# Kernel tuning notes

Hardware: AMD Instinct MI355X
Metric: run time of the kernel (lower is better)

## Reference

```python
import jax, jax.numpy as jnp
import numpy as np

NEG = -1e30  # effective -inf that stays stable in fp32 log-sum-exp
BLANK = 0


def _lse3(a, b, c):
    m = jnp.maximum(jnp.maximum(a, b), c)
    return m + jnp.log(jnp.exp(a - m) + jnp.exp(b - m) + jnp.exp(c - m))


def _ctc_loss_sum(log_probs, input_lengths, targets, target_lengths):
    # log_probs: [B, T, V] already log-softmaxed; targets: [B, S] int, blank=0
    B, T, V = log_probs.shape
    S = targets.shape[1]
    L = 2 * S + 1  # extended label seq: blank-interleaved

    ext = jnp.full((B, L), BLANK, dtype=targets.dtype)
    ext = ext.at[:, 1::2].set(targets)  # [B, L]

    # gather per-frame log-probs of extended labels: [B, T, L]
    lp_ext = jnp.take_along_axis(
        log_probs, jnp.broadcast_to(ext[:, None, :], (B, T, L)), axis=2)

    # skip transition s-2 -> s allowed iff ext[s] != blank and ext[s] != ext[s-2]
    ext_prev2 = jnp.pad(ext[:, :-2], ((0, 0), (2, 0)), constant_values=BLANK)
    can_skip = (ext != BLANK) & (ext != ext_prev2) & (jnp.arange(L)[None, :] >= 2)

    # alpha init at t=0
    alpha = jnp.full((B, L), NEG, dtype=log_probs.dtype)
    alpha = alpha.at[:, 0].set(lp_ext[:, 0, 0])
    alpha = alpha.at[:, 1].set(lp_ext[:, 0, 1])

    lp_seq = jnp.swapaxes(lp_ext, 0, 1)[1:]          # [T-1, B, L]
    valid = jnp.arange(1, T)[:, None] < input_lengths[None, :]  # [T-1, B]

    def step(a, xs):
        lp_t, v = xs  # [B, L], [B]
        a1 = jnp.pad(a[:, :-1], ((0, 0), (1, 0)), constant_values=NEG)
        a2 = jnp.pad(a[:, :-2], ((0, 0), (2, 0)), constant_values=NEG)
        a2 = jnp.where(can_skip, a2, NEG)
        new = _lse3(a, a1, a2) + lp_t
        a = jnp.where(v[:, None], new, a)  # freeze past each utterance's length
        return a, None

    alpha, _ = jax.lax.scan(step, alpha, (lp_seq, valid))

    # terminal states: last blank (2*tl) and last label (2*tl - 1)
    end = 2 * target_lengths.astype(jnp.int32)
    aT = jnp.take_along_axis(alpha, jnp.stack([end, end - 1], axis=1), axis=1)  # [B, 2]
    ll = jax.scipy.special.logsumexp(aT, axis=1)
    loss = -ll
    loss = jnp.where(loss > 1e29, 0.0, loss)  # zero_infinity=True
    return jnp.sum(loss)  # reduction='sum'


def setup_inputs() -> dict:
    B, T, V, S = 64, 1024, 512, 128
    key = jax.random.key(0)
    k1, k2, k3, k4 = jax.random.split(key, 4)
    output_tensor = jax.random.normal(k1, (B, T, V), dtype=jnp.float32)
    output_lengths = jax.random.randint(k2, (B,), T // 2, T + 1, dtype=jnp.int32)
    target_tensor = jax.random.randint(k3, (B, S), 1, V, dtype=jnp.int32)  # no blanks
    target_lengths = jax.random.randint(k4, (B,), S // 2, S + 1, dtype=jnp.int32)
    return {"output_tensor": output_tensor, "output_lengths": output_lengths,
            "target_tensor": target_tensor, "target_lengths": target_lengths}


def reference(output_tensor, output_lengths, target_tensor, target_lengths):
    log_probs = jax.nn.log_softmax(output_tensor, axis=2)
    return _ctc_loss_sum(log_probs, output_lengths, target_tensor, target_lengths)
```

## Files before the change

kernel.cpp:

```cpp
#include <hip/hip_runtime.h>
#include <cstdint>

#define T_LEN 1024
#define V_DIM 512
#define S_LEN 128
#define NEG2  (-1.0e30f)
#define CH    32

__device__ float2 g_plab[(size_t)64 * T_LEN * 64 + 64];
__device__ float  g_pblank[(size_t)64 * T_LEN + 64];

static __device__ __forceinline__ void dma16(const void* g, void* l) {
    __builtin_amdgcn_global_load_lds(
        (const __attribute__((address_space(1))) unsigned int*)g,
        (__attribute__((address_space(3))) unsigned int*)l,
        16, 0, 0);
}

static __device__ __forceinline__ float dpp_shr1_f(float x) {
    return __int_as_float(__builtin_amdgcn_update_dpp(
        0, __float_as_int(x), 0x138, 0xF, 0xF, true));
}
static __device__ __forceinline__ int dpp_shr1_i(int x) {
    return __builtin_amdgcn_update_dpp(0, x, 0x138, 0xF, 0xF, true);
}
template <int CTRL>
static __device__ __forceinline__ float dpp_add(float x) {
    const int y = __builtin_amdgcn_update_dpp(0, __float_as_int(x), CTRL, 0xF, 0xF, true);
    return x + __int_as_float(y);
}

__global__ __launch_bounds__(256) void ctc_prep(
    const float* __restrict__ x, const int* __restrict__ lens,
    const int* __restrict__ tgts)
{
    const int lane = threadIdx.x & 63;
    const int wid  = (int)((blockIdx.x * blockDim.x + threadIdx.x) >> 6);
    const int b = wid >> 10;
    const int t = wid & (T_LEN - 1);
    if (t >= lens[b]) return;

    const float* row = x + (size_t)wid * V_DIM;
    const float4 u = *(const float4*)(row + lane * 8);
    const float4 v = *(const float4*)(row + lane * 8 + 4);

    const float L2E = 1.44269504088896340736f;
    float s = exp2f(u.x * L2E) + exp2f(u.y * L2E)
            + exp2f(u.z * L2E) + exp2f(u.w * L2E)
            + exp2f(v.x * L2E) + exp2f(v.y * L2E)
            + exp2f(v.z * L2E) + exp2f(v.w * L2E);
    s = dpp_add<0x111>(s);
    s = dpp_add<0x112>(s);
    s = dpp_add<0x114>(s);
    s = dpp_add<0x118>(s);
    s = dpp_add<0x142>(s);
    s = dpp_add<0x143>(s);
    const float off =
        log2f(__int_as_float(__builtin_amdgcn_readlane(__float_as_int(s), 63)));

    if (lane == 0) g_pblank[wid] = exp2f(u.x * L2E - off);

    const int2 tg = *(const int2*)(tgts + b * S_LEN + 2 * lane);
    g_plab[(size_t)wid * 64 + lane] =
        make_float2(exp2f(row[tg.x] * L2E - off), exp2f(row[tg.y] * L2E - off));
}

struct AlphaState { float a0, a1, a2, a3, a4; int C; };

static __device__ __forceinline__ void alpha_step(
    AlphaState& st, float pb, float2 lp, float cs1f, float cs3f, bool dead)
{
    const float p3 = dpp_shr1_f(st.a3);
    const int   Cp = dpp_shr1_i(st.C);
    const int   Cn = dead ? Cp : st.C;
    int e = 127 + (Cp - Cn);
    e = e < 0 ? 0 : (e > 252 ? 252 : e);
    const float adj = __int_as_float((unsigned)e << 23);
    const float p3v = p3 * adj;
    const float s01 = st.a0 + st.a1;
    const float s23 = st.a2 + st.a3;
    const float n0 = (st.a0 + p3v) * pb;
    const float n1 = fmaf(p3v, cs1f, s01) * lp.x;
    const float n2 = (st.a1 + st.a2) * pb;
    const float n3 = fmaf(st.a1, cs3f, s23) * lp.y;
    const float n4 = (st.a3 + st.a4) * pb;
    st.a0 = n0; st.a1 = n1; st.a2 = n2; st.a3 = n3; st.a4 = n4; st.C = Cn;
}

static __device__ __forceinline__ void alpha_rescale(AlphaState& st)
{
    const float mx = fmaxf(fmaxf(fmaxf(st.a0, st.a1), fmaxf(st.a2, st.a3)), st.a4);
    const int ee = (__float_as_int(mx) >> 23) & 255;
    const bool ok = (ee > 0) && (ee < 255);
    const float sc = ok ? __int_as_float((unsigned)(254 - ee) << 23) : 1.0f;
    const int dC = ok ? (ee - 127) : 0;
    st.a0 *= sc; st.a1 *= sc; st.a2 *= sc; st.a3 *= sc; st.a4 *= sc; st.C += dC;
}

__global__ __launch_bounds__(64) void ctc_alpha(
    const int* __restrict__ lens, const int* __restrict__ tgts,
    const int* __restrict__ tlens, float* __restrict__ out)
{
    __shared__ alignas(16) float lds_pbs[T_LEN];
    __shared__ float2 lds_pl[3][CH * 64];

    const int b    = blockIdx.x;
    const int lane = threadIdx.x;
    const int len  = lens[b];
    const int tl   = tlens[b];
    const int lenm1 = len - 1;

    const int tA = tgts[b * S_LEN + 2 * lane];
    const int tB = tgts[b * S_LEN + 2 * lane + 1];
    const int tPrev = __shfl_up(tB, 1);
    const bool cs1 = (lane > 0) && (tA != tPrev);
    const bool cs3 = (tB != tA);
    const float cs1f = cs1 ? 1.0f : 0.0f;
    const float cs3f = cs3 ? 1.0f : 0.0f;

    const int repOwn = ((lane > 0 && tA == tPrev) ? 1 : 0) + ((tB == tA) ? 1 : 0);
    int ps = repOwn;
    #pragma unroll
    for (int d = 1; d < 64; d <<= 1) {
        const int y = __shfl_up(ps, d);
        if (lane >= d) ps += y;
    }
    const int deadline = 2 * lane + (ps - repOwn);

    const size_t rowb = (size_t)b * T_LEN;
    const float*  __restrict__ pb_b = g_pblank + rowb;
    const float2* __restrict__ pl_b = g_plab + rowb * 64;

    #pragma unroll
    for (int j = 0; j < CH / 2; ++j)
        dma16(pl_b + (size_t)(1 + 2 * j) * 64 + lane * 2, &lds_pl[0][j * 128]);
    #pragma unroll
    for (int j = 0; j < CH / 2; ++j)
        dma16(pl_b + (size_t)(33 + 2 * j) * 64 + lane * 2, &lds_pl[1][j * 128]);

    #pragma unroll
    for (int k = 0; k < T_LEN / 64; ++k)
        lds_pbs[k * 64 + lane] = pb_b[k * 64 + lane + 1];

    AlphaState st;
    st.a0 = 0.f; st.a1 = 0.f; st.a2 = 0.f; st.a3 = 0.f; st.a4 = 0.f; st.C = 0;
    if (lane == 0) { st.a0 = pb_b[0]; st.a1 = pl_b[0].x; }

    int cur = 0;
    int t0 = 1;
    for (; t0 + CH <= len; t0 += CH) {
        __builtin_amdgcn_s_waitcnt(0x4F70);
        float4 pbq[CH / 4];
        #pragma unroll
        for (int j = 0; j < CH / 4; ++j)
            pbq[j] = *(const float4*)&lds_pbs[(t0 - 1) + 4 * j];
        const float* pbr = (const float*)pbq;
        float2 pl[CH];
        #pragma unroll
        for (int i = 0; i < CH; ++i)
            pl[i] = lds_pl[cur][i * 64 + lane];
        int fill = cur + 2; if (fill >= 3) fill -= 3;
        #pragma unroll
        for (int j = 0; j < CH / 2; ++j) {
            int r = t0 + 2 * CH + 2 * j;
            r = (r < lenm1) ? r : lenm1;
            dma16(pl_b + (size_t)r * 64 + lane * 2, &lds_pl[fill][j * 128]);
        }
        #pragma unroll
        for (int i = 0; i < CH; ++i) {
            const bool dead = (deadline >= t0 + i);
            alpha_step(st, pbr[i], pl[i], cs1f, cs3f, dead);
            if ((i & 3) == 3) alpha_rescale(st);
        }
        cur = (cur == 2) ? 0 : cur + 1;
    }
    __builtin_amdgcn_s_waitcnt(0x0F70);
    for (int i = 0; t0 + i < len; ++i) {
        const float2 plv = lds_pl[cur][i * 64 + lane];
        const float  pb  = lds_pbs[t0 + i - 1];
        const bool dead = (deadline >= t0 + i);
        alpha_step(st, pb, plv, cs1f, cs3f, dead);
        if ((i & 3) == 3) alpha_rescale(st);
    }

    const int end = 2 * tl;
    float v1, v2; int C1, C2;
    {
        int s = end;
        int lsrc = s >> 2; if (lsrc > 63) lsrc = 63;
        const int slot = s & 3;
        float cand = (slot == 0) ? st.a0 : (slot == 1) ? st.a1
                   : (slot == 2) ? st.a2 : st.a3;
        if (s == 256) cand = st.a4;
        v1 = __shfl(cand, lsrc);
        C1 = __shfl(st.C, lsrc);

        s = end - 1;
        lsrc = s >> 2;
        const int slot2 = s & 3;
        cand = (slot2 == 0) ? st.a0 : (slot2 == 1) ? st.a1
             : (slot2 == 2) ? st.a2 : st.a3;
        v2 = __shfl(cand, lsrc);
        C2 = __shfl(st.C, lsrc);
    }
    const float l1 = (v1 > 0.f) ? log2f(v1) + (float)C1 : NEG2;
    const float l2 = (v2 > 0.f) ? log2f(v2) + (float)C2 : NEG2;
    const float mM = fmaxf(l1, l2);
    const float ll2 = mM + log2f(exp2f(l1 - mM) + exp2f(l2 - mM));
    float loss = -ll2 * 0.69314718055994530942f;
    if (!(loss < 1e29f)) loss = 0.f;
    if (lane == 0) atomicAdd(out, loss);
}

extern "C" void kernel_launch(void* const* d_in, const int* in_sizes, int n_in,
                              void* d_out, int out_size, void* d_ws, size_t ws_size,
                              hipStream_t stream) {
    const float* x     = (const float*)d_in[0];
    const int*   lens  = (const int*)d_in[1];
    const int*   tgts  = (const int*)d_in[2];
    const int*   tlens = (const int*)d_in[3];
    float* out = (float*)d_out;

    (void)hipMemsetAsync(d_out, 0, (size_t)out_size * sizeof(float), stream);
    ctc_prep<<<(64 * T_LEN) / 4, 256, 0, stream>>>(x, lens, tgts);
    ctc_alpha<<<64, 64, 0, stream>>>(lens, tgts, tlens, out);
}
```

Measured before the change: 257.0 us.

## Fuse prep and alpha into one producer-consumer kernel with per-group flags

Merges the log-softmax/gather prep kernel and the serial alpha recursion into one launch. The first 64 blocks are consumers that run the CTC recursion, and the remaining blocks are producers that write probabilities in time-major order and bump per-(64-frame group, batch) counters. Consumers spin on these counters before prefetching chunks, so the recursion can overlap with the bandwidth-bound prep instead of waiting for all of it to finish. The blank probabilities are now also streamed per chunk instead of preloaded whole. The cost is an extra memset, atomics and spin-waits. The scheme depends on consumer blocks being scheduled first to avoid deadlock, and on producers finishing in roughly time order.

```diff
diff --git a/kernel.cpp b/kernel.cpp
--- a/kernel.cpp
+++ b/kernel.cpp
@@ -4,11 +4,17 @@
 #define T_LEN 1024
 #define V_DIM 512
 #define S_LEN 128
+#define NB    64
+#define NGRP  16
 #define NEG2  (-1.0e30f)
 #define CH    32
-
-__device__ float2 g_plab[(size_t)64 * T_LEN * 64 + 64];
-__device__ float  g_pblank[(size_t)64 * T_LEN + 64];
+#define CONS_BLOCKS 64
+#define PROD_BLOCKS 16384
+
+__device__ __align__(16) float2 g_plab[(size_t)NB * T_LEN * 64 + 64];
+__device__ __align__(16) float  g_pbs[(size_t)NB * T_LEN + 64];
+__device__ float    g_pb0[NB];
+__device__ unsigned g_flags[NGRP * NB];
 
 static __device__ __forceinline__ void dma16(const void* g, void* l) {
     __builtin_amdgcn_global_load_lds(
@@ -30,17 +36,25 @@
     return x + __int_as_float(y);
 }
 
-__global__ __launch_bounds__(256) void ctc_prep(
+static __device__ __forceinline__ void produce(
     const float* __restrict__ x, const int* __restrict__ lens,
-    const int* __restrict__ tgts)
+    const int* __restrict__ tgts, int pbid)
 {
     const int lane = threadIdx.x & 63;
-    const int wid  = (int)((blockIdx.x * blockDim.x + threadIdx.x) >> 6);
-    const int b = wid >> 10;
-    const int t = wid & (T_LEN - 1);
-    if (t >= lens[b]) return;
-
-    const float* row = x + (size_t)wid * V_DIM;
+    const int wvid = pbid * 4 + (int)(threadIdx.x >> 6);
+    const int t = wvid >> 6;
+    const int b = wvid & (NB - 1);
+    unsigned* flag = &g_flags[(t >> 6) * NB + b];
+
+    if (t >= lens[b]) {
+        if (lane == 0)
+            __hip_atomic_fetch_add(flag, 1u, __ATOMIC_RELAXED,
+                                   __HIP_MEMORY_SCOPE_AGENT);
+        return;
+    }
+
+    const size_t rowid = (size_t)b * T_LEN + t;
+    const float* row = x + rowid * V_DIM;
     const float4 u = *(const float4*)(row + lane * 8);
     const float4 v = *(const float4*)(row + lane * 8 + 4);
 
@@ -58,11 +72,27 @@
     const float off =
         log2f(__int_as_float(__builtin_amdgcn_readlane(__float_as_int(s), 63)));
 
-    if (lane == 0) g_pblank[wid] = exp2f(u.x * L2E - off);
+    if (lane == 0) {
+        const float pv = exp2f(u.x * L2E - off);
+        if (t == 0)
+            __hip_atomic_store(&g_pb0[b], pv, __ATOMIC_RELAXED,
+                               __HIP_MEMORY_SCOPE_AGENT);
+        else
+            __hip_atomic_store(&g_pbs[rowid - 1], pv, __ATOMIC_RELAXED,
+                               __HIP_MEMORY_SCOPE_AGENT);
+    }
 
     const int2 tg = *(const int2*)(tgts + b * S_LEN + 2 * lane);
-    g_plab[(size_t)wid * 64 + lane] =
-        make_float2(exp2f(row[tg.x] * L2E - off), exp2f(row[tg.y] * L2E - off));
+    union { float2 f; unsigned long long q; } cv;
+    cv.f = make_float2(exp2f(row[tg.x] * L2E - off),
+                       exp2f(row[tg.y] * L2E - off));
+    __hip_atomic_store((unsigned long long*)&g_plab[rowid * 64 + lane], cv.q,
+                       __ATOMIC_RELAXED, __HIP_MEMORY_SCOPE_AGENT);
+
+    asm volatile("s_waitcnt vmcnt(0)" ::: "memory");
+    if (lane == 0)
+        __hip_atomic_fetch_add(flag, 1u, __ATOMIC_RELAXED,
+                               __HIP_MEMORY_SCOPE_AGENT);
 }
 
 struct AlphaState { float a0, a1, a2, a3, a4; int C; };
@@ -97,14 +127,26 @@
     st.a0 *= sc; st.a1 *= sc; st.a2 *= sc; st.a3 *= sc; st.a4 *= sc; st.C += dC;
 }
 
-__global__ __launch_bounds__(64) void ctc_alpha(
+static __device__ __forceinline__ void wait_groups(int b, int& gdone, int gneed)
+{
+    if (gneed <= gdone) return;
+    do {
+        ++gdone;
+        while (__hip_atomic_load(&g_flags[gdone * NB + b], __ATOMIC_RELAXED,
+                                 __HIP_MEMORY_SCOPE_AGENT) < 64u)
+            __builtin_amdgcn_s_sleep(2);
+    } while (gdone < gneed);
+    __builtin_amdgcn_fence(__ATOMIC_ACQUIRE, "agent");
+    gdone = gneed;
+}
+
+static __device__ void consume(
     const int* __restrict__ lens, const int* __restrict__ tgts,
-    const int* __restrict__ tlens, float* __restrict__ out)
-{
-    __shared__ alignas(16) float lds_pbs[T_LEN];
-    __shared__ float2 lds_pl[3][CH * 64];
-
-    const int b    = blockIdx.x;
+    const int* __restrict__ tlens, float* __restrict__ out, int b)
+{
+    __shared__ alignas(16) float2 lds_pl[3][CH * 64];
+    __shared__ alignas(16) float  lds_pbc[3][CH];
+
     const int lane = threadIdx.x;
     const int len  = lens[b];
     const int tl   = tlens[b];
@@ -128,37 +170,42 @@
     const int deadline = 2 * lane + (ps - repOwn);
 
     const size_t rowb = (size_t)b * T_LEN;
-    const float*  __restrict__ pb_b = g_pblank + rowb;
-    const float2* __restrict__ pl_b = g_plab + rowb * 64;
+    const float*  __restrict__ pbs_b = g_pbs + rowb;
+    const float2* __restrict__ pl_b  = g_plab + rowb * 64;
+
+    int gdone = -1;
+    wait_groups(b, gdone, 1);
 
     #pragma unroll
     for (int j = 0; j < CH / 2; ++j)
         dma16(pl_b + (size_t)(1 + 2 * j) * 64 + lane * 2, &lds_pl[0][j * 128]);
+    if (lane < 8) dma16(pbs_b + lane * 4, &lds_pbc[0][0]);
     #pragma unroll
     for (int j = 0; j < CH / 2; ++j)
         dma16(pl_b + (size_t)(33 + 2 * j) * 64 + lane * 2, &lds_pl[1][j * 128]);
-
-    #pragma unroll
-    for (int k = 0; k < T_LEN / 64; ++k)
-        lds_pbs[k * 64 + lane] = pb_b[k * 64 + lane + 1];
+    if (lane < 8) dma16(pbs_b + 32 + lane * 4, &lds_pbc[1][0]);
 
     AlphaState st;
     st.a0 = 0.f; st.a1 = 0.f; st.a2 = 0.f; st.a3 = 0.f; st.a4 = 0.f; st.C = 0;
-    if (lane == 0) { st.a0 = pb_b[0]; st.a1 = pl_b[0].x; }
+    if (lane == 0) { st.a0 = g_pb0[b]; st.a1 = pl_b[0].x; }
 
     int cur = 0;
     int t0 = 1;
     for (; t0 + CH <= len; t0 += CH) {
-        __builtin_amdgcn_s_waitcnt(0x4F70);
+        __builtin_amdgcn_s_waitcnt(0x4F71);
         float4 pbq[CH / 4];
         #pragma unroll
         for (int j = 0; j < CH / 4; ++j)
-            pbq[j] = *(const float4*)&lds_pbs[(t0 - 1) + 4 * j];
+            pbq[j] = *(const float4*)&lds_pbc[cur][4 * j];
         const float* pbr = (const float*)pbq;
         float2 pl[CH];
         #pragma unroll
         for (int i = 0; i < CH; ++i)
             pl[i] = lds_pl[cur][i * 64 + lane];
+        {
+            const int gneed = ((t0 + 95 < lenm1) ? t0 + 95 : lenm1) >> 6;
+            wait_groups(b, gdone, gneed);
+        }
         int fill = cur + 2; if (fill >= 3) fill -= 3;
         #pragma unroll
         for (int j = 0; j < CH / 2; ++j) {
@@ -166,6 +213,7 @@
             r = (r < lenm1) ? r : lenm1;
             dma16(pl_b + (size_t)r * 64 + lane * 2, &lds_pl[fill][j * 128]);
         }
+        if (lane < 8) dma16(pbs_b + (t0 + 63) + lane * 4, &lds_pbc[fill][0]);
         #pragma unroll
         for (int i = 0; i < CH; ++i) {
             const bool dead = (deadline >= t0 + i);
@@ -177,7 +225,7 @@
     __builtin_amdgcn_s_waitcnt(0x0F70);
     for (int i = 0; t0 + i < len; ++i) {
         const float2 plv = lds_pl[cur][i * 64 + lane];
-        const float  pb  = lds_pbs[t0 + i - 1];
+        const float  pb  = lds_pbc[cur][i];
         const bool dead = (deadline >= t0 + i);
         alpha_step(st, pb, plv, cs1f, cs3f, dead);
         if ((i & 3) == 3) alpha_rescale(st);
@@ -212,16 +260,34 @@
     if (lane == 0) atomicAdd(out, loss);
 }
 
+__global__ __launch_bounds__(256) void ctc_fused(
+    const float* __restrict__ x, const int* __restrict__ lens,
+    const int* __restrict__ tgts, const int* __restrict__ tlens,
+    float* __restrict__ out)
+{
+    if (blockIdx.x >= CONS_BLOCKS) {
+        produce(x, lens, tgts, (int)blockIdx.x - CONS_BLOCKS);
+        return;
+    }
+    if (threadIdx.x >= 64) return;
+    consume(lens, tgts, tlens, out, (int)blockIdx.x);
+}
+
 extern "C" void kernel_launch(void* const* d_in, const int* in_sizes, int n_in,
                               void* d_out, int out_size, void* d_ws, size_t ws_size,
                               hipStream_t stream) {
+    (void)in_sizes; (void)n_in; (void)d_ws; (void)ws_size;
     const float* x     = (const float*)d_in[0];
     const int*   lens  = (const int*)d_in[1];
     const int*   tgts  = (const int*)d_in[2];
     const int*   tlens = (const int*)d_in[3];
     float* out = (float*)d_out;
 
+    static void* flags_ptr = nullptr;
+    if (!flags_ptr) (void)hipGetSymbolAddress(&flags_ptr, HIP_SYMBOL(g_flags));
+
     (void)hipMemsetAsync(d_out, 0, (size_t)out_size * sizeof(float), stream);
-    ctc_prep<<<(64 * T_LEN) / 4, 256, 0, stream>>>(x, lens, tgts);
-    ctc_alpha<<<64, 64, 0, stream>>>(lens, tgts, tlens, out);
-}
+    (void)hipMemsetAsync(flags_ptr, 0, sizeof(unsigned) * NGRP * NB, stream);
+    ctc_fused<<<CONS_BLOCKS + PROD_BLOCKS, 256, 0, stream>>>(
+        x, lens, tgts, tlens, out);
+}
```

After: 315.2 us. 22.6% more time.
